# Kernel tuning notes

Measured on AMD Instinct MI355X. Metric: run time of the kernel, lower is better.

## Reference

```python
import jax, jax.numpy as jnp
import numpy as np

BN_EPS = 1e-5


def setup_inputs() -> dict:
    key = jax.random.key(0)
    ks = jax.random.split(key, 12)
    B, T, S = 8, 256, 64
    D = 256  # 2*u, u=128
    sc = lambda fan: 1.0 / np.sqrt(fan)
    return {
        "Hx": jax.random.normal(ks[0], (B, T, D), dtype=jnp.float32),
        "Hs": jax.random.normal(ks[1], (S, D), dtype=jnp.float32),
        # transformS = BatchNorm1d(D) -> Linear(D,D) -> ReLU -> Linear(D,D)
        "bn_gamma": jnp.ones((D,), jnp.float32),
        "bn_beta": jnp.zeros((D,), jnp.float32),
        "s_w1": jax.random.normal(ks[2], (D, D), jnp.float32) * sc(D),
        "s_b1": jnp.zeros((D,), jnp.float32),
        "s_w2": jax.random.normal(ks[3], (D, D), jnp.float32) * sc(D),
        "s_b2": jnp.zeros((D,), jnp.float32),
        # W = Linear(3D, D) -> ReLU -> Linear(D, 1)   (6u = 3D features)
        "w_w1": jax.random.normal(ks[4], (3 * D, D), jnp.float32) * sc(3 * D),
        "w_b1": jnp.zeros((D,), jnp.float32),
        "w_w2": jax.random.normal(ks[5], (D, 1), jnp.float32) * sc(D),
        "w_b2": jnp.zeros((1,), jnp.float32),
        "truthSeqY": jax.random.randint(ks[6], (B, T, S), 0, 2, dtype=jnp.int32),
        "inputLen": jax.random.randint(ks[7], (B,), 1, T, dtype=jnp.int32),
    }


def reference(Hx, Hs, bn_gamma, bn_beta, s_w1, s_b1, s_w2, s_b2,
              w_w1, w_b1, w_w2, w_b2, truthSeqY, inputLen):
    B, T, D = Hx.shape
    S = Hs.shape[0]

    # transformS: BatchNorm1d (training-mode batch stats over slot dim) + 2-layer MLP
    mu = jnp.mean(Hs, axis=0)
    var = jnp.var(Hs, axis=0)  # biased, as torch BN uses for normalization
    hs = (Hs - mu) * jax.lax.rsqrt(var + BN_EPS) * bn_gamma + bn_beta
    transHs = jax.nn.relu(hs @ s_w1 + s_b1) @ s_w2 + s_b2  # [S, D]

    # pairwise broadcast: cat(Hx, transHs, Hx*transHs) over [B,T,S,3D]
    mx = jnp.broadcast_to(Hx[:, :, None, :], (B, T, S, D))
    ms = jnp.broadcast_to(transHs[None, None, :, :], (B, T, S, D))
    feat = jnp.concatenate([mx, ms, mx * ms], axis=-1)  # [B,T,S,3D]

    # scoring MLP -> scalar per (token, slot)
    h = jax.nn.relu(feat @ w_w1 + w_b1)        # [B,T,S,D]
    atten = (h @ w_w2 + w_b2)[..., 0]          # [B,T,S]

    atten_score = jax.nn.softmax(atten, axis=2)             # softmax over slots
    G = jnp.einsum('bts,sd->btd', atten_score, transHs)     # weighted slot agg
    outputU = jnp.concatenate([Hx, G + Hx], axis=2)         # [B,T,2D]
    return outputU, atten_score
```

## Files before the change

kernel.cpp:

```cpp
#include <hip/hip_runtime.h>
#include <math.h>

#define DD 256
#define SS 64
#define BT 2048

typedef __attribute__((ext_vector_type(4))) float f32x4;
typedef __attribute__((ext_vector_type(8))) short bf16x8;
typedef __attribute__((ext_vector_type(4))) unsigned int u32x4;

typedef __attribute__((address_space(3))) unsigned lds_u32;
typedef const __attribute__((address_space(1))) unsigned glb_u32;

__device__ inline unsigned pack_bf16(float a, float b) {
    unsigned ua = __builtin_bit_cast(unsigned, a);
    unsigned ub = __builtin_bit_cast(unsigned, b);
    ua = (ua + 0x7fffu + ((ua >> 16) & 1u)) >> 16;
    ub = (ub + 0x7fffu + ((ub >> 16) & 1u)) >> 16;
    return ua | (ub << 16);
}

__global__ __launch_bounds__(1024) void
k_prep2(const float* __restrict__ Hs, const float* __restrict__ g,
        const float* __restrict__ b, const float* __restrict__ s_w1,
        const float* __restrict__ s_b1, const float* __restrict__ s_w2,
        const float* __restrict__ s_b2, const float* __restrict__ w_w1,
        const float* __restrict__ w_b1, float* __restrict__ transHs,
        float* __restrict__ S1b) {
    __shared__ float rowA[DD], rowB[DD], rowC[DD];
    __shared__ float red[8][DD];
    const int s = blockIdx.x;
    const int j = threadIdx.x & 255, kw = threadIdx.x >> 8;
    float sum = 0.f, sumsq = 0.f;
#pragma unroll
    for (int s2 = kw * 16; s2 < kw * 16 + 16; ++s2) {
        float v = Hs[s2 * DD + j];
        sum += v; sumsq += v * v;
    }
    red[kw][j] = sum; red[4 + kw][j] = sumsq;
    __syncthreads();
    if (kw == 0) {
        float st = red[0][j] + red[1][j] + red[2][j] + red[3][j];
        float sq = red[4][j] + red[5][j] + red[6][j] + red[7][j];
        float mu  = st * (1.f / SS);
        float var = sq * (1.f / SS) - mu * mu;
        rowA[j] = (Hs[s * DD + j] - mu) * rsqrtf(var + 1e-5f) * g[j] + b[j];
    }
    __syncthreads();
    float a1 = 0.f;
#pragma unroll 16
    for (int d = kw * 64; d < kw * 64 + 64; ++d)
        a1 = fmaf(rowA[d], s_w1[d * DD + j], a1);
    red[kw][j] = a1;
    __syncthreads();
    if (kw == 0)
        rowB[j] = fmaxf(red[0][j] + red[1][j] + red[2][j] + red[3][j] + s_b1[j], 0.f);
    __syncthreads();
    float a2 = 0.f;
#pragma unroll 16
    for (int d = kw * 64; d < kw * 64 + 64; ++d)
        a2 = fmaf(rowB[d], s_w2[d * DD + j], a2);
    red[kw][j] = a2;
    __syncthreads();
    if (kw == 0) {
        float r = red[0][j] + red[1][j] + red[2][j] + red[3][j] + s_b2[j];
        rowC[j] = r;
        transHs[s * DD + j] = r;
    }
    __syncthreads();
    float a3 = 0.f;
#pragma unroll 16
    for (int d = kw * 64; d < kw * 64 + 64; ++d)
        a3 = fmaf(rowC[d], w_w1[(256 + d) * DD + j], a3);
    red[kw][j] = a3;
    __syncthreads();
    if (kw == 0)
        S1b[s * DD + j] = red[0][j] + red[1][j] + red[2][j] + red[3][j] + w_b1[j];
}

__global__ __launch_bounds__(256) void
k_pack_all(const float* __restrict__ Hx, const float* __restrict__ w_w1,
           const float* __restrict__ transHs, unsigned* __restrict__ Apack,
           unsigned* __restrict__ Bs) {
    const int bid = blockIdx.x;
    if (bid < 256) {
        int idx = bid * 256 + threadIdx.x;
        int lane = idx & 63, ks = (idx >> 6) & 7, MT = idx >> 9;
        int t  = MT * 16 + (lane & 15);
        int k0 = ks * 32 + (lane >> 4) * 8;
        const float* src = Hx + t * DD + k0;
        float4 x0 = *(const float4*)src;
        float4 x1 = *(const float4*)(src + 4);
        unsigned p[4];
        p[0] = pack_bf16(x0.x, x0.y);
        p[1] = pack_bf16(x0.z, x0.w);
        p[2] = pack_bf16(x1.x, x1.y);
        p[3] = pack_bf16(x1.z, x1.w);
        *(u32x4*)(Apack + idx * 4) = *(const u32x4*)p;
    } else {
        int b2 = bid - 256;
        int s = b2 >> 5;
        int idx = (b2 & 31) * 256 + threadIdx.x;
        int lane = idx & 63, ks = (idx >> 6) & 7, nt = idx >> 9;
        int j  = nt * 16 + (lane & 15);
        int k0 = ks * 32 + (lane >> 4) * 8;
        const float* C   = w_w1 + 512 * DD;
        const float* W1a = w_w1;
        const float* ms  = transHs + s * DD;
        unsigned p[4];
#pragma unroll
        for (int e = 0; e < 4; ++e) {
            int k = k0 + 2 * e;
            float f0 = W1a[k * DD + j] + ms[k] * C[k * DD + j];
            float f1 = W1a[(k + 1) * DD + j] + ms[k + 1] * C[(k + 1) * DD + j];
            p[e] = pack_bf16(f0, f1);
        }
        *(u32x4*)(Bs + (s * 8192 + idx) * 4) = *(const u32x4*)p;
    }
}

__global__ __launch_bounds__(256, 2) void
k_main_mfma(const unsigned* __restrict__ Apack, const unsigned* __restrict__ Bs,
            const float* __restrict__ S1b, const float* __restrict__ w2,
            const float* __restrict__ w_b2, float* __restrict__ atten) {
    __shared__ unsigned Albs[16384];
    const int s  = blockIdx.y;
    const int t0 = blockIdx.x * 128;
    const int tid = threadIdx.x;
    const int w = tid >> 6, l = tid & 63;
    const int lrow = l & 15, lg = l >> 4;
    const unsigned* Asrc = Apack + blockIdx.x * 16384;
    const unsigned* Bsl  = Bs + s * 32768;

#pragma unroll
    for (int i = 0; i < 16; ++i) {
        int chunk = w * 16 + i;
        __builtin_amdgcn_global_load_lds((glb_u32*)(Asrc + chunk * 256 + l * 4),
                                         (lds_u32*)(Albs + chunk * 256), 16, 0, 0);
    }
    __syncthreads();

    f32x4 acc[8][4] = {};
    for (int ks = 0; ks < 8; ++ks) {
        bf16x8 af[8];
#pragma unroll
        for (int mt = 0; mt < 8; ++mt)
            af[mt] = *(const bf16x8*)((const char*)Albs + ((mt * 8 + ks) * 64 + l) * 16);
#pragma unroll
        for (int nt = 0; nt < 4; ++nt) {
            const bf16x8 bf = *(const bf16x8*)(Bsl + (((w * 4 + nt) * 8 + ks) * 64 + l) * 4);
#pragma unroll
            for (int mt = 0; mt < 8; ++mt)
                acc[mt][nt] = __builtin_amdgcn_mfma_f32_16x16x32_bf16(af[mt], bf, acc[mt][nt], 0, 0, 0);
        }
    }
    __syncthreads();

    float* attp = (float*)Albs;
    float s1[4], w2v[4];
#pragma unroll
    for (int nt = 0; nt < 4; ++nt) {
        int jn = (w * 4 + nt) * 16 + lrow;
        s1[nt]  = S1b[s * DD + jn];
        w2v[nt] = w2[jn];
    }
#pragma unroll
    for (int mt = 0; mt < 8; ++mt) {
#pragma unroll
        for (int i = 0; i < 4; ++i) {
            float p = 0.f;
#pragma unroll
            for (int nt = 0; nt < 4; ++nt) {
                float h = fmaxf(acc[mt][nt][i] + s1[nt], 0.f);
                p = fmaf(h, w2v[nt], p);
            }
            p += __shfl_xor(p, 1);
            p += __shfl_xor(p, 2);
            p += __shfl_xor(p, 4);
            p += __shfl_xor(p, 8);
            if (lrow == 0) attp[w * 128 + mt * 16 + lg * 4 + i] = p;
        }
    }
    __syncthreads();
    if (tid < 128) {
        float r = attp[tid] + attp[128 + tid] + attp[256 + tid] + attp[384 + tid] + w_b2[0];
        atten[(t0 + tid) * SS + s] = r;
    }
}

__global__ __launch_bounds__(256) void
k_out(const float* __restrict__ Hx, const float* __restrict__ m,
      const float* __restrict__ atten, float* __restrict__ outU,
      float* __restrict__ outA) {
    int wave = threadIdx.x >> 6, lane = threadIdx.x & 63;
    int t = blockIdx.x * 4 + wave;
    float a = atten[t * SS + lane];
    float mx = a;
#pragma unroll
    for (int off = 32; off; off >>= 1) mx = fmaxf(mx, __shfl_xor(mx, off));
    float e = __expf(a - mx);
    float sum = e;
#pragma unroll
    for (int off = 32; off; off >>= 1) sum += __shfl_xor(sum, off);
    float p = e / sum;
    outA[t * SS + lane] = p;
    float gacc[4] = {};
    for (int s = 0; s < SS; ++s) {
        float ps = __shfl(p, s);
#pragma unroll
        for (int q = 0; q < 4; ++q)
            gacc[q] = fmaf(ps, m[s * DD + lane + 64 * q], gacc[q]);
    }
#pragma unroll
    for (int q = 0; q < 4; ++q) {
        int j = lane + 64 * q;
        float x = Hx[t * DD + j];
        outU[t * 2 * DD + j] = x;
        outU[t * 2 * DD + DD + j] = x + gacc[q];
    }
}

extern "C" void kernel_launch(void* const* d_in, const int* in_sizes, int n_in,
                              void* d_out, int out_size, void* d_ws, size_t ws_size,
                              hipStream_t stream) {
    const float* Hx   = (const float*)d_in[0];
    const float* Hs   = (const float*)d_in[1];
    const float* bn_g = (const float*)d_in[2];
    const float* bn_b = (const float*)d_in[3];
    const float* s_w1 = (const float*)d_in[4];
    const float* s_b1 = (const float*)d_in[5];
    const float* s_w2 = (const float*)d_in[6];
    const float* s_b2 = (const float*)d_in[7];
    const float* w_w1 = (const float*)d_in[8];
    const float* w_b1 = (const float*)d_in[9];
    const float* w_w2 = (const float*)d_in[10];
    const float* w_b2 = (const float*)d_in[11];

    float* ws      = (float*)d_ws;
    float* transHs = ws;
    float* S1b     = ws + 16384;
    float* atten   = ws + 32768;
    unsigned* Apack = (unsigned*)(ws + 163840);
    unsigned* Bs    = Apack + 262144;

    float* outU = (float*)d_out;
    float* outA = outU + BT * 2 * DD;

    k_prep2<<<SS, 1024, 0, stream>>>(Hs, bn_g, bn_b, s_w1, s_b1, s_w2, s_b2,
                                     w_w1, w_b1, transHs, S1b);
    k_pack_all<<<2304, 256, 0, stream>>>(Hx, w_w1, transHs, Apack, Bs);
    dim3 gmain(BT / 128, SS);
    k_main_mfma<<<gmain, 256, 0, stream>>>(Apack, Bs, S1b, w_w2, w_b2, atten);
    k_out<<<BT / 4, 256, 0, stream>>>(Hx, transHs, atten, outU, outA);
}
```

Baseline: 61.13 us.

## Split pack kernel, reuse weights across slots, swizzle main-kernel block order

The B-operand pack now loads the w_w1 and C weight values once per thread into registers and reuses them across 16 slots, with transHs staged in LDS. Before, each of the 64 slot-blocks re-read the weights from global memory. The A pack becomes its own kernel, which adds one launch. The main MFMA kernel uses a 1D grid with a swizzled block-to-(slot, tile) mapping to change cache locality, and its k-loop is fully unrolled. The bs kernel now has only 128 blocks, which lowers parallelism, and the extra unroll may raise register pressure.

```diff
diff --git a/kernel.cpp b/kernel.cpp
--- a/kernel.cpp
+++ b/kernel.cpp
@@ -79,43 +79,55 @@
 }
 
 __global__ __launch_bounds__(256) void
-k_pack_all(const float* __restrict__ Hx, const float* __restrict__ w_w1,
-           const float* __restrict__ transHs, unsigned* __restrict__ Apack,
-           unsigned* __restrict__ Bs) {
-    const int bid = blockIdx.x;
-    if (bid < 256) {
-        int idx = bid * 256 + threadIdx.x;
-        int lane = idx & 63, ks = (idx >> 6) & 7, MT = idx >> 9;
-        int t  = MT * 16 + (lane & 15);
-        int k0 = ks * 32 + (lane >> 4) * 8;
-        const float* src = Hx + t * DD + k0;
-        float4 x0 = *(const float4*)src;
-        float4 x1 = *(const float4*)(src + 4);
+k_pack_a(const float* __restrict__ Hx, unsigned* __restrict__ Apack) {
+    int idx = blockIdx.x * 256 + threadIdx.x;
+    int lane = idx & 63, ks = (idx >> 6) & 7, MT = idx >> 9;
+    int t  = MT * 16 + (lane & 15);
+    int k0 = ks * 32 + (lane >> 4) * 8;
+    const float* src = Hx + t * DD + k0;
+    float4 x0 = *(const float4*)src;
+    float4 x1 = *(const float4*)(src + 4);
+    unsigned p[4];
+    p[0] = pack_bf16(x0.x, x0.y);
+    p[1] = pack_bf16(x0.z, x0.w);
+    p[2] = pack_bf16(x1.x, x1.y);
+    p[3] = pack_bf16(x1.z, x1.w);
+    *(u32x4*)(Apack + idx * 4) = *(const u32x4*)p;
+}
+
+__global__ __launch_bounds__(256) void
+k_pack_bs(const float* __restrict__ w_w1, const float* __restrict__ transHs,
+          unsigned* __restrict__ Bs) {
+    __shared__ float ms_l[16][DD];
+    const int ic = blockIdx.x & 31, sg = blockIdx.x >> 5;
+    const int s0 = sg * 16;
+    const int tid = threadIdx.x;
+#pragma unroll
+    for (int i = 0; i < 4; ++i) {
+        int e4 = i * 256 + tid;
+        ((float4*)ms_l)[e4] = ((const float4*)(transHs + s0 * DD))[e4];
+    }
+    __syncthreads();
+    const int idx = ic * 256 + tid;
+    const int lane = idx & 63, ks = (idx >> 6) & 7, nt = idx >> 9;
+    const int j  = nt * 16 + (lane & 15);
+    const int k0 = ks * 32 + (lane >> 4) * 8;
+    const float* C   = w_w1 + 512 * DD;
+    float w1v[8], cv[8];
+#pragma unroll
+    for (int e = 0; e < 8; ++e) {
+        w1v[e] = w_w1[(k0 + e) * DD + j];
+        cv[e]  = C[(k0 + e) * DD + j];
+    }
+    for (int ss = 0; ss < 16; ++ss) {
         unsigned p[4];
-        p[0] = pack_bf16(x0.x, x0.y);
-        p[1] = pack_bf16(x0.z, x0.w);
-        p[2] = pack_bf16(x1.x, x1.y);
-        p[3] = pack_bf16(x1.z, x1.w);
-        *(u32x4*)(Apack + idx * 4) = *(const u32x4*)p;
-    } else {
-        int b2 = bid - 256;
-        int s = b2 >> 5;
-        int idx = (b2 & 31) * 256 + threadIdx.x;
-        int lane = idx & 63, ks = (idx >> 6) & 7, nt = idx >> 9;
-        int j  = nt * 16 + (lane & 15);
-        int k0 = ks * 32 + (lane >> 4) * 8;
-        const float* C   = w_w1 + 512 * DD;
-        const float* W1a = w_w1;
-        const float* ms  = transHs + s * DD;
-        unsigned p[4];
 #pragma unroll
         for (int e = 0; e < 4; ++e) {
-            int k = k0 + 2 * e;
-            float f0 = W1a[k * DD + j] + ms[k] * C[k * DD + j];
-            float f1 = W1a[(k + 1) * DD + j] + ms[k + 1] * C[(k + 1) * DD + j];
+            float f0 = w1v[2 * e]     + ms_l[ss][k0 + 2 * e]     * cv[2 * e];
+            float f1 = w1v[2 * e + 1] + ms_l[ss][k0 + 2 * e + 1] * cv[2 * e + 1];
             p[e] = pack_bf16(f0, f1);
         }
-        *(u32x4*)(Bs + (s * 8192 + idx) * 4) = *(const u32x4*)p;
+        *(u32x4*)(Bs + ((s0 + ss) * 8192 + idx) * 4) = *(const u32x4*)p;
     }
 }
 
@@ -124,12 +136,14 @@
             const float* __restrict__ S1b, const float* __restrict__ w2,
             const float* __restrict__ w_b2, float* __restrict__ atten) {
     __shared__ unsigned Albs[16384];
-    const int s  = blockIdx.y;
-    const int t0 = blockIdx.x * 128;
+    const int swz  = (blockIdx.x & 7) * 128 + (blockIdx.x >> 3);
+    const int s    = swz >> 4;
+    const int tile = swz & 15;
+    const int t0 = tile * 128;
     const int tid = threadIdx.x;
     const int w = tid >> 6, l = tid & 63;
     const int lrow = l & 15, lg = l >> 4;
-    const unsigned* Asrc = Apack + blockIdx.x * 16384;
+    const unsigned* Asrc = Apack + tile * 16384;
     const unsigned* Bsl  = Bs + s * 32768;
 
 #pragma unroll
@@ -141,6 +155,7 @@
     __syncthreads();
 
     f32x4 acc[8][4] = {};
+#pragma unroll
     for (int ks = 0; ks < 8; ++ks) {
         bf16x8 af[8];
 #pragma unroll
@@ -248,8 +263,8 @@
 
     k_prep2<<<SS, 1024, 0, stream>>>(Hs, bn_g, bn_b, s_w1, s_b1, s_w2, s_b2,
                                      w_w1, w_b1, transHs, S1b);
-    k_pack_all<<<2304, 256, 0, stream>>>(Hx, w_w1, transHs, Apack, Bs);
-    dim3 gmain(BT / 128, SS);
-    k_main_mfma<<<gmain, 256, 0, stream>>>(Apack, Bs, S1b, w_w2, w_b2, atten);
+    k_pack_a<<<256, 256, 0, stream>>>(Hx, Apack);
+    k_pack_bs<<<128, 256, 0, stream>>>(w_w1, transHs, Bs);
+    k_main_mfma<<<1024, 256, 0, stream>>>(Apack, Bs, S1b, w_w2, w_b2, atten);
     k_out<<<BT / 4, 256, 0, stream>>>(Hx, transHs, atten, outU, outA);
 }
```

New measurement: 61.26 us. About the same (+0.2%).
